# Performance work log

Hardware: AMD Instinct MI355X
Metric: run time of the kernel (lower is better)

Reference implementation:

```python
import jax, jax.numpy as jnp
import numpy as np

EPS = 1e-8


def setup_inputs() -> dict:
    key = jax.random.key(0)
    ks = jax.random.split(key, 11)
    N, D_OBS, D_AC, K = 2_000_000, 32, 16, 128
    H = int(1.66 * K)  # 212, matches int(1.66*k) in the torch module
    s = 0.05
    return {
        "obs": jax.random.normal(ks[0], (N, D_OBS), dtype=jnp.float32),
        "acs": jax.random.normal(ks[1], (N, D_AC), dtype=jnp.float32),
        "x": jax.random.normal(ks[2], (D_OBS,), dtype=jnp.float32),
        "w_in": jax.random.normal(ks[3], (H, K), dtype=jnp.float32) * s,
        "b_in": jax.random.normal(ks[4], (H,), dtype=jnp.float32) * s,
        "w2": jax.random.normal(ks[5], (H, H), dtype=jnp.float32) * s,
        "b2": jax.random.normal(ks[6], (H,), dtype=jnp.float32) * s,
        "w3": jax.random.normal(ks[7], (H, H), dtype=jnp.float32) * s,
        "b3": jax.random.normal(ks[8], (H,), dtype=jnp.float32) * s,
        "w_out": jax.random.normal(ks[9], (K, H), dtype=jnp.float32) * s,
        "b_out": jax.random.normal(ks[10], (K,), dtype=jnp.float32) * s,
        "k": K,
    }


def reference(obs, acs, x, w_in, b_in, w2, b2, w3, b3, w_out, b_out, k):
    # cosine distance between every obs row and the query x: [N]
    xn = x * jax.lax.rsqrt(jnp.sum(x * x) + EPS)
    obs_nrm = jax.lax.rsqrt(jnp.sum(obs * obs, axis=1) + EPS)  # [N]
    cos_sim = (obs @ xn) * obs_nrm                              # [N]
    cos_dist = 1.0 - cos_sim                                    # [N]

    # top-k smallest distances (argpartition equivalent, sorted ascending)
    neg_vals, idx = jax.lax.top_k(-cos_dist, k)                 # [k], [k]
    k_cos_dist = -neg_vals                                      # [k]
    k_actions = acs[idx]                                        # [k, D_ac]

    # tiny MLP on the k distances -> softmax weights over the k neighbors
    h = jax.nn.relu(k_cos_dist @ w_in.T + b_in)
    h = jax.nn.relu(h @ w2.T + b2)
    h = jax.nn.relu(h @ w3.T + b3)
    weights = jax.nn.softmax(h @ w_out.T + b_out)               # [k]

    # weighted sum of the k neighbor actions -> [1, D_ac]
    out = jnp.sum(weights[:, None] * k_actions, axis=0, keepdims=True)
    return out
```

## Files before the change

kernel.cpp:

```cpp
#include <hip/hip_runtime.h>
#include <math.h>

#define NBIN 4096
#define CAPC 4096
#define KSEL 128
#define HDIM 212
#define DAC  16
#define EPSF 1e-8f
#define GRID1 2048

__global__ void k_init(const float* __restrict__ x, float* __restrict__ xn,
                       unsigned* __restrict__ hist, unsigned* __restrict__ meta) {
    int t = threadIdx.x;
    __shared__ float rs;
    if (t < 32) {
        float v = x[t];
        float s = v * v;
        #pragma unroll
        for (int o = 16; o >= 1; o >>= 1) s += __shfl_down(s, o);
        if (t == 0) rs = rsqrtf(s + EPSF);
    }
    __syncthreads();
    if (t < 32) xn[t] = x[t] * rs;
    for (int b = t; b < NBIN; b += blockDim.x) hist[b] = 0u;
    if (t < 8) meta[t] = 0u;
}

__global__ __launch_bounds__(256) void k_cos_hist(
        const float4* __restrict__ obs4, const float* __restrict__ xn,
        float* __restrict__ cosb, unsigned* __restrict__ hist, int N) {
    __shared__ unsigned lhist[NBIN];
    __shared__ float xs[32];
    for (int b = threadIdx.x; b < NBIN; b += 256) lhist[b] = 0u;
    if (threadIdx.x < 32) xs[threadIdx.x] = xn[threadIdx.x];
    __syncthreads();

    float4 X[8];
    #pragma unroll
    for (int q = 0; q < 8; q++)
        X[q] = make_float4(xs[4*q+0], xs[4*q+1], xs[4*q+2], xs[4*q+3]);

    const int stride = gridDim.x * blockDim.x;
    int row = blockIdx.x * blockDim.x + threadIdx.x;

    #define D4(v, q) ((v).x*X[q].x + (v).y*X[q].y + (v).z*X[q].z + (v).w*X[q].w)
    #define N4(v)    ((v).x*(v).x + (v).y*(v).y + (v).z*(v).z + (v).w*(v).w)

    for (; row + stride < N; row += 2*stride) {
        const float4* ra = obs4 + (size_t)row * 8;
        const float4* rb = obs4 + (size_t)(row + stride) * 8;
        float4 a0 = ra[0], a1 = ra[1], a2 = ra[2], a3 = ra[3];
        float4 a4 = ra[4], a5 = ra[5], a6 = ra[6], a7 = ra[7];
        float4 b0 = rb[0], b1 = rb[1], b2 = rb[2], b3 = rb[3];
        float4 b4 = rb[4], b5 = rb[5], b6 = rb[6], b7 = rb[7];

        float dotA = (D4(a0,0) + D4(a1,1)) + (D4(a2,2) + D4(a3,3))
                   + (D4(a4,4) + D4(a5,5)) + (D4(a6,6) + D4(a7,7));
        float nrmA = (N4(a0) + N4(a1)) + (N4(a2) + N4(a3))
                   + (N4(a4) + N4(a5)) + (N4(a6) + N4(a7));
        float dotB = (D4(b0,0) + D4(b1,1)) + (D4(b2,2) + D4(b3,3))
                   + (D4(b4,4) + D4(b5,5)) + (D4(b6,6) + D4(b7,7));
        float nrmB = (N4(b0) + N4(b1)) + (N4(b2) + N4(b3))
                   + (N4(b4) + N4(b5)) + (N4(b6) + N4(b7));

        float cdA = 1.0f - dotA * rsqrtf(nrmA + EPSF);
        float cdB = 1.0f - dotB * rsqrtf(nrmB + EPSF);
        cosb[row] = cdA;
        cosb[row + stride] = cdB;
        unsigned uA = __float_as_uint(cdA);
        unsigned kA = (uA & 0x80000000u) ? ~uA : (uA | 0x80000000u);
        unsigned uB = __float_as_uint(cdB);
        unsigned kB = (uB & 0x80000000u) ? ~uB : (uB | 0x80000000u);
        atomicAdd(&lhist[kA >> 20], 1u);
        atomicAdd(&lhist[kB >> 20], 1u);
    }
    for (; row < N; row += stride) {
        const float4* rp = obs4 + (size_t)row * 8;
        float4 a0 = rp[0], a1 = rp[1], a2 = rp[2], a3 = rp[3];
        float4 a4 = rp[4], a5 = rp[5], a6 = rp[6], a7 = rp[7];
        float dot = (D4(a0,0) + D4(a1,1)) + (D4(a2,2) + D4(a3,3))
                  + (D4(a4,4) + D4(a5,5)) + (D4(a6,6) + D4(a7,7));
        float nrm = (N4(a0) + N4(a1)) + (N4(a2) + N4(a3))
                  + (N4(a4) + N4(a5)) + (N4(a6) + N4(a7));
        float cd = 1.0f - dot * rsqrtf(nrm + EPSF);
        cosb[row] = cd;
        unsigned u = __float_as_uint(cd);
        unsigned key = (u & 0x80000000u) ? ~u : (u | 0x80000000u);
        atomicAdd(&lhist[key >> 20], 1u);
    }
    #undef D4
    #undef N4

    __syncthreads();
    for (int b = threadIdx.x; b < NBIN; b += 256) {
        unsigned c = lhist[b];
        if (c) atomicAdd(&hist[b], c);
    }
}

__global__ __launch_bounds__(64) void k_scan(const unsigned* __restrict__ hist,
                                             unsigned* __restrict__ meta, int K) {
    int t = threadIdx.x;
    unsigned c[64];
    unsigned local = 0;
    #pragma unroll
    for (int q = 0; q < 64; q++) { c[q] = hist[64*t + q]; local += c[q]; }
    unsigned sc = local;
    #pragma unroll
    for (int o = 1; o < 64; o <<= 1) {
        unsigned v = __shfl_up(sc, o);
        if (t >= o) sc += v;
    }
    unsigned incl = sc, excl = sc - local;
    if (excl < (unsigned)K && (unsigned)K <= incl) {
        unsigned cum = excl;
        int B = 64*t;
        for (int q = 0; q < 64; q++) {
            cum += c[q];
            if (cum >= (unsigned)K) { B = 64*t + q; break; }
        }
        meta[1] = (B >= NBIN - 1) ? 0xFFFFFFFFu : ((unsigned)(B + 1) << 20);
    }
}

__global__ __launch_bounds__(256) void k_compact(
        const float4* __restrict__ cos4, unsigned* __restrict__ meta,
        float* __restrict__ cval, int* __restrict__ cidx, int n4, int N) {
    unsigned keyHi = meta[1];
    int g = blockIdx.x * blockDim.x + threadIdx.x;
    if (g >= n4) return;
    float4 v = cos4[g];
    float vv[4] = {v.x, v.y, v.z, v.w};
    #pragma unroll
    for (int q = 0; q < 4; q++) {
        int i = g*4 + q;
        if (i < N) {
            unsigned u = __float_as_uint(vv[q]);
            unsigned key = (u & 0x80000000u) ? ~u : (u | 0x80000000u);
            if (key < keyHi) {
                unsigned pos = atomicAdd(&meta[0], 1u);
                if (pos < CAPC) { cval[pos] = vv[q]; cidx[pos] = i; }
            }
        }
    }
}

__global__ __launch_bounds__(512) void k_final(
        const float* __restrict__ cval, const int* __restrict__ cidx,
        const unsigned* __restrict__ meta, const float* __restrict__ acs,
        const float* __restrict__ w_in, const float* __restrict__ b_in,
        const float* __restrict__ w2, const float* __restrict__ b2,
        const float* __restrict__ w3, const float* __restrict__ b3,
        const float* __restrict__ w_out, const float* __restrict__ b_out,
        float* __restrict__ out) {
    __shared__ unsigned kv[CAPC];
    __shared__ int      idv[CAPC];
    __shared__ unsigned char act[CAPC];
    __shared__ unsigned hist2[256];
    __shared__ unsigned remArr[9];
    __shared__ unsigned pivB[8];
    __shared__ unsigned selB_sh;
    __shared__ unsigned scnt;
    __shared__ unsigned skey[KSEL];
    __shared__ int      sidx[KSEL];
    __shared__ float    sval[KSEL];
    __shared__ float d[KSEL];
    __shared__ int   id2[KSEL];
    __shared__ float h1[HDIM], h2[HDIM], h3[HDIM], lg[KSEL];
    __shared__ float smax_sh, rsum_sh;

    const int t = threadIdx.x;
    int M = (int)meta[0];
    if (M > CAPC) M = CAPC;

    for (int i = t; i < M; i += 512) {
        float v = cval[i];
        unsigned u = __float_as_uint(v);
        kv[i]  = (u & 0x80000000u) ? ~u : (u | 0x80000000u);
        idv[i] = cidx[i];
        act[i] = 1;
    }
    if (t == 0) remArr[0] = KSEL - 1;
    if (t < KSEL) {
        skey[t] = 0xFFFFFFFFu; sidx[t] = 0x7FFFFFFF; sval[t] = 0.f;
        d[t] = 0.f; id2[t] = 0;
    }
    __syncthreads();

    for (int r = 0; r < 8; r++) {
        if (t < 256) hist2[t] = 0u;
        __syncthreads();
        for (int i = t; i < M; i += 512) {
            if (act[i]) {
                unsigned b = (r < 4) ? ((kv[i] >> ((3-r)*8)) & 0xFFu)
                                     : (((unsigned)idv[i] >> ((7-r)*8)) & 0xFFu);
                atomicAdd(&hist2[b], 1u);
            }
        }
        __syncthreads();
        if (t < 64) {
            unsigned s0 = hist2[4*t], s1 = hist2[4*t+1],
                     s2 = hist2[4*t+2], s3 = hist2[4*t+3];
            unsigned tot = s0 + s1 + s2 + s3;
            unsigned sc = tot;
            #pragma unroll
            for (int o = 1; o < 64; o <<= 1) {
                unsigned v2 = __shfl_up(sc, o);
                if (t >= o) sc += v2;
            }
            unsigned cb = sc - tot;
            unsigned rm = remArr[r];
            unsigned ss[4] = {s0, s1, s2, s3};
            #pragma unroll
            for (int q = 0; q < 4; q++) {
                if (cb <= rm && rm < cb + ss[q]) {
                    selB_sh = 4*t + q;
                    pivB[r] = 4*t + q;
                    remArr[r+1] = rm - cb;
                }
                cb += ss[q];
            }
        }
        __syncthreads();
        unsigned sb = selB_sh;
        for (int i = t; i < M; i += 512) {
            if (act[i]) {
                unsigned b = (r < 4) ? ((kv[i] >> ((3-r)*8)) & 0xFFu)
                                     : (((unsigned)idv[i] >> ((7-r)*8)) & 0xFFu);
                if (b != sb) act[i] = 0;
            }
        }
        __syncthreads();
    }

    unsigned kvP = (pivB[0]<<24) | (pivB[1]<<16) | (pivB[2]<<8) | pivB[3];
    unsigned idP = (pivB[4]<<24) | (pivB[5]<<16) | (pivB[6]<<8) | pivB[7];
    if (t == 0) scnt = 0u;
    __syncthreads();

    for (int i = t; i < M; i += 512) {
        unsigned k = kv[i];
        unsigned ui = (unsigned)idv[i];
        if (k < kvP || (k == kvP && ui <= idP)) {
            unsigned p = atomicAdd(&scnt, 1u);
            if (p < KSEL) {
                skey[p] = k;
                sidx[p] = idv[i];
                unsigned u = (k & 0x80000000u) ? (k & 0x7FFFFFFFu) : ~k;
                sval[p] = __uint_as_float(u);
            }
        }
    }
    __syncthreads();

    if (t < KSEL) {
        unsigned mk = skey[t], mi = (unsigned)sidx[t];
        int rank = 0;
        for (int j = 0; j < KSEL; j++) {
            unsigned jk = skey[j], ji = (unsigned)sidx[j];
            rank += (jk < mk || (jk == mk && ji < mi)) ? 1 : 0;
        }
        d[rank] = sval[t];
        id2[rank] = sidx[t];
    }
    __syncthreads();

    if (t < HDIM) {
        float s = b_in[t];
        const float* wr = &w_in[t * KSEL];
        for (int j = 0; j < KSEL; j++) s += wr[j] * d[j];
        h1[t] = s > 0.f ? s : 0.f;
    }
    __syncthreads();
    if (t < HDIM) {
        float s = b2[t];
        const float* wr = &w2[t * HDIM];
        for (int j = 0; j < HDIM; j++) s += wr[j] * h1[j];
        h2[t] = s > 0.f ? s : 0.f;
    }
    __syncthreads();
    if (t < HDIM) {
        float s = b3[t];
        const float* wr = &w3[t * HDIM];
        for (int j = 0; j < HDIM; j++) s += wr[j] * h2[j];
        h3[t] = s > 0.f ? s : 0.f;
    }
    __syncthreads();
    if (t < KSEL) {
        float s = b_out[t];
        const float* wr = &w_out[t * HDIM];
        for (int j = 0; j < HDIM; j++) s += wr[j] * h3[j];
        lg[t] = s;
    }
    __syncthreads();

    if (t < 64) {
        float a = fmaxf(lg[t], lg[t + 64]);
        #pragma unroll
        for (int o = 32; o >= 1; o >>= 1) a = fmaxf(a, __shfl_xor(a, o));
        if (t == 0) smax_sh = a;
    }
    __syncthreads();
    if (t < KSEL) lg[t] = __expf(lg[t] - smax_sh);
    __syncthreads();
    if (t < 64) {
        float s = lg[t] + lg[t + 64];
        #pragma unroll
        for (int o = 32; o >= 1; o >>= 1) s += __shfl_xor(s, o);
        if (t == 0) rsum_sh = 1.0f / s;
    }
    __syncthreads();

    if (t < DAC) {
        float s = 0.f;
        for (int j = 0; j < KSEL; j++)
            s += lg[j] * acs[(size_t)id2[j] * DAC + t];
        out[t] = s * rsum_sh;
    }
}

extern "C" void kernel_launch(void* const* d_in, const int* in_sizes, int n_in,
                              void* d_out, int out_size, void* d_ws, size_t ws_size,
                              hipStream_t stream) {
    const float* obs   = (const float*)d_in[0];
    const float* acs   = (const float*)d_in[1];
    const float* x     = (const float*)d_in[2];
    const float* w_in  = (const float*)d_in[3];
    const float* b_in  = (const float*)d_in[4];
    const float* w2    = (const float*)d_in[5];
    const float* b2    = (const float*)d_in[6];
    const float* w3    = (const float*)d_in[7];
    const float* b3    = (const float*)d_in[8];
    const float* w_out = (const float*)d_in[9];
    const float* b_out = (const float*)d_in[10];
    float* out = (float*)d_out;

    int N = in_sizes[0] / 32;

    char* ws = (char*)d_ws;
    float*    xn   = (float*)ws;
    float*    cosb = (float*)(ws + 256);
    size_t histOff = 256 + (((size_t)N * 4 + 255) / 256) * 256;
    unsigned* hist = (unsigned*)(ws + histOff);
    unsigned* meta = (unsigned*)(ws + histOff + NBIN * 4);
    float*    cval = (float*)(ws + histOff + NBIN * 4 + 256);
    int*      cidx = (int*)(ws + histOff + NBIN * 4 + 256 + CAPC * 4);

    k_init<<<1, 256, 0, stream>>>(x, xn, hist, meta);

    k_cos_hist<<<GRID1, 256, 0, stream>>>((const float4*)obs, xn, cosb, hist, N);

    k_scan<<<1, 64, 0, stream>>>(hist, meta, KSEL);

    int n4 = (N + 3) / 4;
    k_compact<<<(n4 + 255) / 256, 256, 0, stream>>>((const float4*)cosb, meta,
                                                    cval, cidx, n4, N);

    k_final<<<1, 512, 0, stream>>>(cval, cidx, meta, acs, w_in, b_in,
                                   w2, b2, w3, b3, w_out, b_out, out);
}
```

Before: 165.5 us.

## Stage obs tiles into LDS via global_load_lds with swizzled layout

The cosine/histogram kernel no longer has each thread read its own 128-byte row directly from global memory. Each block now pulls 256-row tiles into LDS with direct global-to-LDS 16-byte loads, which are coalesced across lanes, and uses an XOR swizzle so the per-row reads from LDS avoid bank conflicts. The goal is better global access coalescing. In exchange it adds 32KB of LDS per block, which may lower occupancy, and two barriers per tile with no double-buffering, so load latency is not overlapped with compute. The two-rows-per-iteration unroll is also dropped.

```diff
diff --git a/kernel.cpp b/kernel.cpp
--- a/kernel.cpp
+++ b/kernel.cpp
@@ -8,6 +8,14 @@
 #define DAC  16
 #define EPSF 1e-8f
 #define GRID1 2048
+#define TROWS 256
+#define TBYTES (TROWS * 128)
+
+__device__ __forceinline__ void gload_lds16(const void* g, void* l) {
+    __builtin_amdgcn_global_load_lds(
+        (const __attribute__((address_space(1))) unsigned int*)g,
+        (__attribute__((address_space(3))) unsigned int*)l, 16, 0, 0);
+}
 
 __global__ void k_init(const float* __restrict__ x, float* __restrict__ xn,
                        unsigned* __restrict__ hist, unsigned* __restrict__ meta) {
@@ -27,9 +35,10 @@
 }
 
 __global__ __launch_bounds__(256) void k_cos_hist(
-        const float4* __restrict__ obs4, const float* __restrict__ xn,
+        const char* __restrict__ obs, const float* __restrict__ xn,
         float* __restrict__ cosb, unsigned* __restrict__ hist, int N) {
     __shared__ unsigned lhist[NBIN];
+    __shared__ char tile[TBYTES];
     __shared__ float xs[32];
     for (int b = threadIdx.x; b < NBIN; b += 256) lhist[b] = 0u;
     if (threadIdx.x < 32) xs[threadIdx.x] = xn[threadIdx.x];
@@ -40,53 +49,57 @@
     for (int q = 0; q < 8; q++)
         X[q] = make_float4(xs[4*q+0], xs[4*q+1], xs[4*q+2], xs[4*q+3]);
 
-    const int stride = gridDim.x * blockDim.x;
-    int row = blockIdx.x * blockDim.x + threadIdx.x;
+    const int t = threadIdx.x;
+    const int wave = t >> 6, lane = t & 63;
+    const int fullTiles = N / TROWS;
 
     #define D4(v, q) ((v).x*X[q].x + (v).y*X[q].y + (v).z*X[q].z + (v).w*X[q].w)
     #define N4(v)    ((v).x*(v).x + (v).y*(v).y + (v).z*(v).z + (v).w*(v).w)
 
-    for (; row + stride < N; row += 2*stride) {
-        const float4* ra = obs4 + (size_t)row * 8;
-        const float4* rb = obs4 + (size_t)(row + stride) * 8;
-        float4 a0 = ra[0], a1 = ra[1], a2 = ra[2], a3 = ra[3];
-        float4 a4 = ra[4], a5 = ra[5], a6 = ra[6], a7 = ra[7];
-        float4 b0 = rb[0], b1 = rb[1], b2 = rb[2], b3 = rb[3];
-        float4 b4 = rb[4], b5 = rb[5], b6 = rb[6], b7 = rb[7];
-
-        float dotA = (D4(a0,0) + D4(a1,1)) + (D4(a2,2) + D4(a3,3))
-                   + (D4(a4,4) + D4(a5,5)) + (D4(a6,6) + D4(a7,7));
-        float nrmA = (N4(a0) + N4(a1)) + (N4(a2) + N4(a3))
-                   + (N4(a4) + N4(a5)) + (N4(a6) + N4(a7));
-        float dotB = (D4(b0,0) + D4(b1,1)) + (D4(b2,2) + D4(b3,3))
-                   + (D4(b4,4) + D4(b5,5)) + (D4(b6,6) + D4(b7,7));
-        float nrmB = (N4(b0) + N4(b1)) + (N4(b2) + N4(b3))
-                   + (N4(b4) + N4(b5)) + (N4(b6) + N4(b7));
-
-        float cdA = 1.0f - dotA * rsqrtf(nrmA + EPSF);
-        float cdB = 1.0f - dotB * rsqrtf(nrmB + EPSF);
-        cosb[row] = cdA;
-        cosb[row + stride] = cdB;
-        unsigned uA = __float_as_uint(cdA);
-        unsigned kA = (uA & 0x80000000u) ? ~uA : (uA | 0x80000000u);
-        unsigned uB = __float_as_uint(cdB);
-        unsigned kB = (uB & 0x80000000u) ? ~uB : (uB | 0x80000000u);
-        atomicAdd(&lhist[kA >> 20], 1u);
-        atomicAdd(&lhist[kB >> 20], 1u);
-    }
-    for (; row < N; row += stride) {
-        const float4* rp = obs4 + (size_t)row * 8;
-        float4 a0 = rp[0], a1 = rp[1], a2 = rp[2], a3 = rp[3];
-        float4 a4 = rp[4], a5 = rp[5], a6 = rp[6], a7 = rp[7];
-        float dot = (D4(a0,0) + D4(a1,1)) + (D4(a2,2) + D4(a3,3))
-                  + (D4(a4,4) + D4(a5,5)) + (D4(a6,6) + D4(a7,7));
-        float nrm = (N4(a0) + N4(a1)) + (N4(a2) + N4(a3))
-                  + (N4(a4) + N4(a5)) + (N4(a6) + N4(a7));
+    for (int tl = blockIdx.x; tl < fullTiles; tl += gridDim.x) {
+        const char* gbase = obs + (size_t)tl * TBYTES;
+        #pragma unroll
+        for (int i = 0; i < 8; i++) {
+            int dst = wave * 8192 + i * 1024;
+            int o   = dst + lane * 16;
+            int src = o ^ (((o >> 7) & 7) << 4);
+            gload_lds16(gbase + src, tile + dst);
+        }
+        __syncthreads();
+
+        const int xr = (t & 7) << 4;
+        const char* rbase = tile + t * 128;
+        #define RD(q) (*(const float4*)(rbase + (((q) * 16) ^ xr)))
+        float4 v0 = RD(0), v1 = RD(1), v2 = RD(2), v3 = RD(3);
+        float4 v4 = RD(4), v5 = RD(5), v6 = RD(6), v7 = RD(7);
+        #undef RD
+        float dot = (D4(v0,0) + D4(v1,1)) + (D4(v2,2) + D4(v3,3))
+                  + (D4(v4,4) + D4(v5,5)) + (D4(v6,6) + D4(v7,7));
+        float nrm = (N4(v0) + N4(v1)) + (N4(v2) + N4(v3))
+                  + (N4(v4) + N4(v5)) + (N4(v6) + N4(v7));
         float cd = 1.0f - dot * rsqrtf(nrm + EPSF);
-        cosb[row] = cd;
+        cosb[tl * TROWS + t] = cd;
         unsigned u = __float_as_uint(cd);
         unsigned key = (u & 0x80000000u) ? ~u : (u | 0x80000000u);
         atomicAdd(&lhist[key >> 20], 1u);
+        __syncthreads();
+    }
+
+    if (blockIdx.x == gridDim.x - 1) {
+        for (int row = fullTiles * TROWS + t; row < N; row += 256) {
+            const float4* rp = (const float4*)(obs + (size_t)row * 128);
+            float4 v0 = rp[0], v1 = rp[1], v2 = rp[2], v3 = rp[3];
+            float4 v4 = rp[4], v5 = rp[5], v6 = rp[6], v7 = rp[7];
+            float dot = (D4(v0,0) + D4(v1,1)) + (D4(v2,2) + D4(v3,3))
+                      + (D4(v4,4) + D4(v5,5)) + (D4(v6,6) + D4(v7,7));
+            float nrm = (N4(v0) + N4(v1)) + (N4(v2) + N4(v3))
+                      + (N4(v4) + N4(v5)) + (N4(v6) + N4(v7));
+            float cd = 1.0f - dot * rsqrtf(nrm + EPSF);
+            cosb[row] = cd;
+            unsigned u = __float_as_uint(cd);
+            unsigned key = (u & 0x80000000u) ? ~u : (u | 0x80000000u);
+            atomicAdd(&lhist[key >> 20], 1u);
+        }
     }
     #undef D4
     #undef N4
@@ -348,7 +361,7 @@
 
     k_init<<<1, 256, 0, stream>>>(x, xn, hist, meta);
 
-    k_cos_hist<<<GRID1, 256, 0, stream>>>((const float4*)obs, xn, cosb, hist, N);
+    k_cos_hist<<<GRID1, 256, 0, stream>>>((const char*)obs, xn, cosb, hist, N);
 
     k_scan<<<1, 64, 0, stream>>>(hist, meta, KSEL);
 
```

Result: faster. 136.7 us (-17.4%).

## Split cosine and histogram kernels; coalesce obs reads with 8-lane shuffle reduction

Applied to the files above, without the earlier changes.

The fused cosine+histogram kernel becomes two kernels. The cosine kernel gives each row's eight float4s to eight adjacent lanes, so obs loads are fully coalesced, and reduces the dot product and norm with xor shuffles. A separate histogram kernel rereads the distance buffer and aggregates equal bins per wavefront with ballot/leader before each shared atomic, which cuts contention. The cost is an extra launch, an extra 8MB read of the distance buffer, and three shuffle rounds per float4.

```diff
diff --git a/kernel.cpp b/kernel.cpp
--- a/kernel.cpp
+++ b/kernel.cpp
@@ -26,71 +26,62 @@
     if (t < 8) meta[t] = 0u;
 }
 
-__global__ __launch_bounds__(256) void k_cos_hist(
+__global__ __launch_bounds__(256) void k_cos(
         const float4* __restrict__ obs4, const float* __restrict__ xn,
-        float* __restrict__ cosb, unsigned* __restrict__ hist, int N) {
+        float* __restrict__ cosb, long total8) {
+    __shared__ float xs[32];
+    if (threadIdx.x < 32) xs[threadIdx.x] = xn[threadIdx.x];
+    __syncthreads();
+    const int r = threadIdx.x & 7;
+    const float c0 = xs[4*r+0], c1 = xs[4*r+1], c2 = xs[4*r+2], c3 = xs[4*r+3];
+
+    const long stride = (long)gridDim.x * blockDim.x;
+    long g = (long)blockIdx.x * blockDim.x + threadIdx.x;
+
+    #define BODY(G) do {                                                  \
+        float4 v = obs4[(G)];                                             \
+        float dot = v.x*c0 + v.y*c1 + v.z*c2 + v.w*c3;                    \
+        float nrm = v.x*v.x + v.y*v.y + v.z*v.z + v.w*v.w;                \
+        dot += __shfl_xor(dot, 1); nrm += __shfl_xor(nrm, 1);             \
+        dot += __shfl_xor(dot, 2); nrm += __shfl_xor(nrm, 2);             \
+        dot += __shfl_xor(dot, 4); nrm += __shfl_xor(nrm, 4);             \
+        if (r == 0) cosb[(G) >> 3] = 1.0f - dot * rsqrtf(nrm + EPSF);     \
+    } while (0)
+
+    for (; g + stride < total8; g += 2*stride) {
+        BODY(g);
+        BODY(g + stride);
+    }
+    for (; g < total8; g += stride) BODY(g);
+    #undef BODY
+}
+
+__global__ __launch_bounds__(256) void k_hist(
+        const float* __restrict__ cosb, unsigned* __restrict__ hist, int N) {
     __shared__ unsigned lhist[NBIN];
-    __shared__ float xs[32];
     for (int b = threadIdx.x; b < NBIN; b += 256) lhist[b] = 0u;
-    if (threadIdx.x < 32) xs[threadIdx.x] = xn[threadIdx.x];
-    __syncthreads();
-
-    float4 X[8];
-    #pragma unroll
-    for (int q = 0; q < 8; q++)
-        X[q] = make_float4(xs[4*q+0], xs[4*q+1], xs[4*q+2], xs[4*q+3]);
-
+    __syncthreads();
+
+    const int lane = threadIdx.x & 63;
     const int stride = gridDim.x * blockDim.x;
-    int row = blockIdx.x * blockDim.x + threadIdx.x;
-
-    #define D4(v, q) ((v).x*X[q].x + (v).y*X[q].y + (v).z*X[q].z + (v).w*X[q].w)
-    #define N4(v)    ((v).x*(v).x + (v).y*(v).y + (v).z*(v).z + (v).w*(v).w)
-
-    for (; row + stride < N; row += 2*stride) {
-        const float4* ra = obs4 + (size_t)row * 8;
-        const float4* rb = obs4 + (size_t)(row + stride) * 8;
-        float4 a0 = ra[0], a1 = ra[1], a2 = ra[2], a3 = ra[3];
-        float4 a4 = ra[4], a5 = ra[5], a6 = ra[6], a7 = ra[7];
-        float4 b0 = rb[0], b1 = rb[1], b2 = rb[2], b3 = rb[3];
-        float4 b4 = rb[4], b5 = rb[5], b6 = rb[6], b7 = rb[7];
-
-        float dotA = (D4(a0,0) + D4(a1,1)) + (D4(a2,2) + D4(a3,3))
-                   + (D4(a4,4) + D4(a5,5)) + (D4(a6,6) + D4(a7,7));
-        float nrmA = (N4(a0) + N4(a1)) + (N4(a2) + N4(a3))
-                   + (N4(a4) + N4(a5)) + (N4(a6) + N4(a7));
-        float dotB = (D4(b0,0) + D4(b1,1)) + (D4(b2,2) + D4(b3,3))
-                   + (D4(b4,4) + D4(b5,5)) + (D4(b6,6) + D4(b7,7));
-        float nrmB = (N4(b0) + N4(b1)) + (N4(b2) + N4(b3))
-                   + (N4(b4) + N4(b5)) + (N4(b6) + N4(b7));
-
-        float cdA = 1.0f - dotA * rsqrtf(nrmA + EPSF);
-        float cdB = 1.0f - dotB * rsqrtf(nrmB + EPSF);
-        cosb[row] = cdA;
-        cosb[row + stride] = cdB;
-        unsigned uA = __float_as_uint(cdA);
-        unsigned kA = (uA & 0x80000000u) ? ~uA : (uA | 0x80000000u);
-        unsigned uB = __float_as_uint(cdB);
-        unsigned kB = (uB & 0x80000000u) ? ~uB : (uB | 0x80000000u);
-        atomicAdd(&lhist[kA >> 20], 1u);
-        atomicAdd(&lhist[kB >> 20], 1u);
-    }
-    for (; row < N; row += stride) {
-        const float4* rp = obs4 + (size_t)row * 8;
-        float4 a0 = rp[0], a1 = rp[1], a2 = rp[2], a3 = rp[3];
-        float4 a4 = rp[4], a5 = rp[5], a6 = rp[6], a7 = rp[7];
-        float dot = (D4(a0,0) + D4(a1,1)) + (D4(a2,2) + D4(a3,3))
-                  + (D4(a4,4) + D4(a5,5)) + (D4(a6,6) + D4(a7,7));
-        float nrm = (N4(a0) + N4(a1)) + (N4(a2) + N4(a3))
-                  + (N4(a4) + N4(a5)) + (N4(a6) + N4(a7));
-        float cd = 1.0f - dot * rsqrtf(nrm + EPSF);
-        cosb[row] = cd;
-        unsigned u = __float_as_uint(cd);
-        unsigned key = (u & 0x80000000u) ? ~u : (u | 0x80000000u);
-        atomicAdd(&lhist[key >> 20], 1u);
-    }
-    #undef D4
-    #undef N4
-
+    for (int i = blockIdx.x * blockDim.x + threadIdx.x; ; i += stride) {
+        bool p = (i < N);
+        unsigned long long mask = __ballot(p);
+        if (!mask) break;
+        unsigned bin = 0;
+        if (p) {
+            unsigned u = __float_as_uint(cosb[i]);
+            unsigned key = (u & 0x80000000u) ? ~u : (u | 0x80000000u);
+            bin = key >> 20;
+        }
+        while (mask) {
+            int leader = __ffsll((unsigned long long)mask) - 1;
+            unsigned lb = (unsigned)__shfl((int)bin, leader);
+            unsigned long long eq = __ballot(bin == lb) & mask;
+            if (lane == leader) atomicAdd(&lhist[lb], (unsigned)__popcll(eq));
+            mask &= ~eq;
+        }
+    }
     __syncthreads();
     for (int b = threadIdx.x; b < NBIN; b += 256) {
         unsigned c = lhist[b];
@@ -348,7 +339,10 @@
 
     k_init<<<1, 256, 0, stream>>>(x, xn, hist, meta);
 
-    k_cos_hist<<<GRID1, 256, 0, stream>>>((const float4*)obs, xn, cosb, hist, N);
+    long total8 = (long)N * 8;
+    k_cos<<<GRID1, 256, 0, stream>>>((const float4*)obs, xn, cosb, total8);
+
+    k_hist<<<512, 256, 0, stream>>>(cosb, hist, N);
 
     k_scan<<<1, 64, 0, stream>>>(hist, meta, KSEL);
 
```

New measurement: 156.6 us. 5.4% less time.
